# Kernel tuning notes

Hardware: AMD Instinct MI355X
Metric: run time of the kernel (lower is better)

Reference implementation:

```python
import jax, jax.numpy as jnp
import numpy as np

N_NODES = 50000
N_EDGES = 1600000
IN_C, HID_C, OUT_C = 64, 64, 7


def setup_inputs() -> dict:
    key = jax.random.key(0)
    ks = jax.random.split(key, 8)
    x = jax.random.normal(ks[0], (N_NODES, IN_C), dtype=jnp.float32)
    edge_index = jax.random.randint(ks[1], (2, N_EDGES), 0, N_NODES, dtype=jnp.int64)
    s_in = 1.0 / np.sqrt(IN_C)
    s_hid = 1.0 / np.sqrt(HID_C)
    W1 = jax.random.normal(ks[2], (HID_C, IN_C), dtype=jnp.float32) * s_in
    b1 = jnp.zeros((HID_C,), dtype=jnp.float32)
    W2 = jax.random.normal(ks[3], (HID_C, HID_C), dtype=jnp.float32) * s_hid
    b2 = jnp.zeros((HID_C,), dtype=jnp.float32)
    W3 = jax.random.normal(ks[4], (OUT_C, HID_C), dtype=jnp.float32) * s_hid
    b3 = jnp.zeros((OUT_C,), dtype=jnp.float32)
    return {"x": x, "edge_index": edge_index, "W1": W1, "b1": b1,
            "W2": W2, "b2": b2, "W3": W3, "b3": b3}


def _gcn_conv(x, src, dst, W, b):
    # GCNConv(normalize=False): lin -> sum-aggregate over incoming edges -> +bias
    h = x @ W.T                                   # [N, out]
    msg = h[src]                                  # gather source features [E, out]
    agg = jax.ops.segment_sum(msg, dst, num_segments=N_NODES)  # scatter-add
    return agg + b


def reference(x, edge_index, W1, b1, W2, b2, W3, b3):
    src, dst = edge_index[0], edge_index[1]
    h = jax.nn.relu(_gcn_conv(x, src, dst, W1, b1))   # dropout is identity in eval
    h = jax.nn.relu(_gcn_conv(h, src, dst, W2, b2))
    h = _gcn_conv(h, src, dst, W3, b3)
    return jax.nn.log_softmax(h, axis=-1)
```

## Files before the change

### kernel.cpp

```cpp
#include <hip/hip_runtime.h>
#include <math.h>

#define N_NODES 50000
#define N_EDGES 1600000
#define C 64
#define OUTC 7

#define NB 196
#define BCAP 10240
#define CHUNK 8192

#define ZROW N_NODES

typedef __attribute__((ext_vector_type(8))) short bf16x8;
typedef __attribute__((ext_vector_type(4))) float f32x4;
typedef __attribute__((ext_vector_type(2))) float f32x2;

__device__ __forceinline__ unsigned int pk_bf16(float a, float b) {
    unsigned int ua = __float_as_uint(a);
    ua = (ua + 0x7FFFu + ((ua >> 16) & 1u)) >> 16;
    unsigned int ub = __float_as_uint(b);
    ub = (ub + 0x7FFFu + ((ub >> 16) & 1u)) >> 16;
    return ua | (ub << 16);
}

union U4B8 { uint4 u; bf16x8 s; };

__global__ __launch_bounds__(256) void prep(const float* __restrict__ W1,
                                            const float* __restrict__ W2,
                                            unsigned int* __restrict__ Wb1,
                                            unsigned int* __restrict__ Wb2,
                                            int* __restrict__ gcursor) {
    const int b = blockIdx.x;
    const int tid = threadIdx.x;
    if (b < 8) {
        int idx = b * 256 + tid;
        float2 v = ((const float2*)W1)[idx];
        Wb1[idx] = pk_bf16(v.x, v.y);
    } else if (b < 16) {
        int idx = (b - 8) * 256 + tid;
        float2 v = ((const float2*)W2)[idx];
        Wb2[idx] = pk_bf16(v.x, v.y);
    } else {
        if (tid < NB) gcursor[tid] = 0;
    }
}

__global__ __launch_bounds__(256) void bin_kernel(const int* __restrict__ src,
                                                  const int* __restrict__ dst,
                                                  unsigned int* __restrict__ buckets,
                                                  int* __restrict__ gcursor) {
    __shared__ unsigned int staged[CHUNK];
    __shared__ int hist[NB], scanb[NB], cur[NB], baseb[NB];
    const int tid = threadIdx.x;
    const int base = blockIdx.x * CHUNK;
    int n = N_EDGES - base; if (n > CHUNK) n = CHUNK;

    for (int b = tid; b < NB; b += 256) { hist[b] = 0; cur[b] = 0; }
    __syncthreads();

    const int4* src4 = (const int4*)(src + base);
    const int4* dst4 = (const int4*)(dst + base);
    unsigned int v[32];
    int nv = n >> 2;
#pragma unroll
    for (int k = 0; k < 8; ++k) {
        int i4 = k * 256 + tid;
        if (i4 < nv) {
            int4 s4 = src4[i4];
            int4 d4 = dst4[i4];
            unsigned int d0 = (unsigned int)d4.x, d1 = (unsigned int)d4.y;
            unsigned int d2 = (unsigned int)d4.z, d3 = (unsigned int)d4.w;
            v[k * 4 + 0] = (d0 << 16) | (unsigned int)s4.x;
            v[k * 4 + 1] = (d1 << 16) | (unsigned int)s4.y;
            v[k * 4 + 2] = (d2 << 16) | (unsigned int)s4.z;
            v[k * 4 + 3] = (d3 << 16) | (unsigned int)s4.w;
            atomicAdd(&hist[d0 >> 8], 1);
            atomicAdd(&hist[d1 >> 8], 1);
            atomicAdd(&hist[d2 >> 8], 1);
            atomicAdd(&hist[d3 >> 8], 1);
        }
    }
    __syncthreads();
    if (tid == 0) {
        int run = 0;
        for (int b = 0; b < NB; ++b) { scanb[b] = run; run += hist[b]; }
    }
    __syncthreads();
#pragma unroll
    for (int k = 0; k < 8; ++k) {
        int i4 = k * 256 + tid;
        if (i4 < nv) {
#pragma unroll
            for (int q = 0; q < 4; ++q) {
                unsigned int w = v[k * 4 + q];
                int b = w >> 24;
                int p = scanb[b] + atomicAdd(&cur[b], 1);
                staged[p] = w;
            }
        }
    }
    __syncthreads();
    if (tid < NB) baseb[tid] = atomicAdd(&gcursor[tid], hist[tid]);
    __syncthreads();
    for (int i = tid; i < n; i += 256) {
        unsigned int w = staged[i];
        int b = w >> 24;
        buckets[(size_t)b * BCAP + baseb[b] + (i - scanb[b])] = w;
    }
}

__global__ __launch_bounds__(256) void build_csr(const unsigned int* __restrict__ buckets,
                                                 const int* __restrict__ gcursor,
                                                 unsigned int* __restrict__ csr,
                                                 int* __restrict__ off) {
    __shared__ int hist[256], part[256], offx[256], cur[256];
    __shared__ int gl[NB];
    __shared__ int s_cnt, s_base;
    const int tid = threadIdx.x;
    const int b = blockIdx.x;

    hist[tid] = 0;
    cur[tid] = 0;
    if (tid < NB) gl[tid] = gcursor[tid];
    __syncthreads();
    if (tid == 0) {
        int bs = 0;
        for (int i = 0; i < b; ++i) bs += gl[i];
        s_base = bs;
        s_cnt = gl[b];
    }
    __syncthreads();
    const int cnt = s_cnt;
    const int gbase = s_base;
    const unsigned int* bk = buckets + (size_t)b * BCAP;

    for (int i = tid; i < cnt; i += 256) {
        atomicAdd(&hist[(bk[i] >> 16) & 255], 1);
    }
    __syncthreads();
    part[tid] = hist[tid];
    __syncthreads();
    for (int d = 1; d < 256; d <<= 1) {
        int t = (tid >= d) ? part[tid - d] : 0;
        __syncthreads();
        part[tid] += t;
        __syncthreads();
    }
    offx[tid] = (tid == 0) ? 0 : part[tid - 1];
    __syncthreads();
    int node = b * 256 + tid;
    if (node < N_NODES) off[node] = gbase + offx[tid];
    if (b == NB - 1 && tid == 0) off[N_NODES] = gbase + cnt;
    for (int i = tid; i < cnt; i += 256) {
        unsigned int w = bk[i];
        int dl = (w >> 16) & 255;
        int p = offx[dl] + atomicAdd(&cur[dl], 1);
        csr[gbase + p] = w & 0xFFFFu;
    }
}


__global__ __launch_bounds__(256) void linear64_mfma_x(const float* __restrict__ x,
                                                       const unsigned int* __restrict__ Wb,
                                                       unsigned int* __restrict__ out) {
    if (blockIdx.x == 0 && threadIdx.x < 32)
        out[(size_t)ZROW * 32 + threadIdx.x] = 0u;
    const int wave = threadIdx.x >> 6;
    const int lane = threadIdx.x & 63;
    const int quad = lane >> 4;
    const int l16  = lane & 15;
    const int rbase = blockIdx.x * 64 + wave * 16;
    if (rbase >= N_NODES) return;

    U4B8 bfrag[4][2];
#pragma unroll
    for (int ct = 0; ct < 4; ++ct)
#pragma unroll
        for (int kt = 0; kt < 2; ++kt)
            bfrag[ct][kt].u = *(const uint4*)(Wb + (ct * 16 + l16) * 32 + kt * 16 + quad * 4);

    U4B8 afrag[2];
#pragma unroll
    for (int kt = 0; kt < 2; ++kt) {
        const float4* xp = (const float4*)(x + (size_t)(rbase + l16) * 64 + kt * 32 + quad * 8);
        float4 f0 = xp[0];
        float4 f1 = xp[1];
        afrag[kt].u.x = pk_bf16(f0.x, f0.y);
        afrag[kt].u.y = pk_bf16(f0.z, f0.w);
        afrag[kt].u.z = pk_bf16(f1.x, f1.y);
        afrag[kt].u.w = pk_bf16(f1.z, f1.w);
    }

    f32x4 acc[4];
#pragma unroll
    for (int ct = 0; ct < 4; ++ct) {
        f32x4 z = {0.f, 0.f, 0.f, 0.f};
        z = __builtin_amdgcn_mfma_f32_16x16x32_bf16(afrag[0].s, bfrag[ct][0].s, z, 0, 0, 0);
        z = __builtin_amdgcn_mfma_f32_16x16x32_bf16(afrag[1].s, bfrag[ct][1].s, z, 0, 0, 0);
        acc[ct] = z;
    }

    const int colp = l16 >> 1;
    const bool even = (l16 & 1) == 0;
#pragma unroll
    for (int ct = 0; ct < 4; ++ct) {
#pragma unroll
        for (int i = 0; i < 4; ++i) {
            float v = acc[ct][i];
            float p = __shfl_xor(v, 1, 64);
            if (even) {
                int row = rbase + quad * 4 + i;
                out[(size_t)row * 32 + ct * 8 + colp] = pk_bf16(v, p);
            }
        }
    }
}

__global__ __launch_bounds__(256) void linear64_mfma(const unsigned int* __restrict__ in,
                                                     const unsigned int* __restrict__ Wb,
                                                     unsigned int* __restrict__ out) {
    if (blockIdx.x == 0 && threadIdx.x < 32)
        out[(size_t)ZROW * 32 + threadIdx.x] = 0u;
    const int wave = threadIdx.x >> 6;
    const int lane = threadIdx.x & 63;
    const int quad = lane >> 4;
    const int l16  = lane & 15;
    const int rbase = blockIdx.x * 64 + wave * 16;
    if (rbase >= N_NODES) return;

    U4B8 bfrag[4][2];
#pragma unroll
    for (int ct = 0; ct < 4; ++ct)
#pragma unroll
        for (int kt = 0; kt < 2; ++kt)
            bfrag[ct][kt].u = *(const uint4*)(Wb + (ct * 16 + l16) * 32 + kt * 16 + quad * 4);

    U4B8 afrag[2];
#pragma unroll
    for (int kt = 0; kt < 2; ++kt)
        afrag[kt].u = *(const uint4*)(in + (size_t)(rbase + l16) * 32 + kt * 16 + quad * 4);

    f32x4 acc[4];
#pragma unroll
    for (int ct = 0; ct < 4; ++ct) {
        f32x4 z = {0.f, 0.f, 0.f, 0.f};
        z = __builtin_amdgcn_mfma_f32_16x16x32_bf16(afrag[0].s, bfrag[ct][0].s, z, 0, 0, 0);
        z = __builtin_amdgcn_mfma_f32_16x16x32_bf16(afrag[1].s, bfrag[ct][1].s, z, 0, 0, 0);
        acc[ct] = z;
    }

    const int colp = l16 >> 1;
    const bool even = (l16 & 1) == 0;
#pragma unroll
    for (int ct = 0; ct < 4; ++ct) {
#pragma unroll
        for (int i = 0; i < 4; ++i) {
            float v = acc[ct][i];
            float p = __shfl_xor(v, 1, 64);
            if (even) {
                int row = rbase + quad * 4 + i;
                out[(size_t)row * 32 + ct * 8 + colp] = pk_bf16(v, p);
            }
        }
    }
}

#define ACC8(v)                                                              \
    do {                                                                     \
        s01 += (f32x2){__uint_as_float((v).x << 16),                         \
                       __uint_as_float((v).x & 0xFFFF0000u)};                \
        s23 += (f32x2){__uint_as_float((v).y << 16),                         \
                       __uint_as_float((v).y & 0xFFFF0000u)};                \
        s45 += (f32x2){__uint_as_float((v).z << 16),                         \
                       __uint_as_float((v).z & 0xFFFF0000u)};                \
        s67 += (f32x2){__uint_as_float((v).w << 16),                         \
                       __uint_as_float((v).w & 0xFFFF0000u)};                \
    } while (0)

__global__ __launch_bounds__(256) void gather64b(const int* __restrict__ off,
                                                 const unsigned int* __restrict__ csr_src,
                                                 const unsigned int* __restrict__ tb,
                                                 const float* __restrict__ b,
                                                 unsigned int* __restrict__ hb) {
    int node = blockIdx.x * 4 + (threadIdx.x >> 6);
    if (node >= N_NODES) return;
    const int lane = threadIdx.x & 63;
    const int slot = lane >> 3;
    const int ch8  = lane & 7;
    int e0 = off[node], e1 = off[node + 1];
    const uint4* t4 = (const uint4*)tb;
    f32x2 s01 = {0.f, 0.f}, s23 = {0.f, 0.f}, s45 = {0.f, 0.f}, s67 = {0.f, 0.f};
    for (int e = e0; e < e1; e += 32) {
        int i0 = e + slot, i1 = i0 + 8, i2 = i0 + 16, i3 = i0 + 24;
        unsigned int a0 = csr_src[i0];
        unsigned int a1 = csr_src[i1];
        unsigned int a2 = csr_src[i2];
        unsigned int a3 = csr_src[i3];
        a0 = (i0 < e1) ? a0 : ZROW;
        a1 = (i1 < e1) ? a1 : ZROW;
        a2 = (i2 < e1) ? a2 : ZROW;
        a3 = (i3 < e1) ? a3 : ZROW;
        uint4 v0 = t4[(size_t)a0 * 8 + ch8];
        uint4 v1 = t4[(size_t)a1 * 8 + ch8];
        uint4 v2 = t4[(size_t)a2 * 8 + ch8];
        uint4 v3 = t4[(size_t)a3 * 8 + ch8];
        ACC8(v0);
        ACC8(v1);
        ACC8(v2);
        ACC8(v3);
    }
    float s[8] = {s01.x, s01.y, s23.x, s23.y, s45.x, s45.y, s67.x, s67.y};
#pragma unroll
    for (int d = 8; d <= 32; d <<= 1) {
#pragma unroll
        for (int j = 0; j < 8; ++j) s[j] += __shfl_xor(s[j], d, 64);
    }
    if (lane < 8) {
        const float4 b0 = ((const float4*)b)[ch8 * 2];
        const float4 b1 = ((const float4*)b)[ch8 * 2 + 1];
        float r0 = fmaxf(s[0] + b0.x, 0.f);
        float r1 = fmaxf(s[1] + b0.y, 0.f);
        float r2 = fmaxf(s[2] + b0.z, 0.f);
        float r3 = fmaxf(s[3] + b0.w, 0.f);
        float r4 = fmaxf(s[4] + b1.x, 0.f);
        float r5 = fmaxf(s[5] + b1.y, 0.f);
        float r6 = fmaxf(s[6] + b1.z, 0.f);
        float r7 = fmaxf(s[7] + b1.w, 0.f);
        uint4 w;
        w.x = pk_bf16(r0, r1);
        w.y = pk_bf16(r2, r3);
        w.z = pk_bf16(r4, r5);
        w.w = pk_bf16(r6, r7);
        ((uint4*)(hb + (size_t)node * 32))[ch8] = w;
    }
}

__global__ __launch_bounds__(256) void gather64b_w3(const int* __restrict__ off,
                                                    const unsigned int* __restrict__ csr_src,
                                                    const unsigned int* __restrict__ tb,
                                                    const float* __restrict__ b,
                                                    const float* __restrict__ W3,
                                                    unsigned int* __restrict__ t3) {
    int node = blockIdx.x * 4 + (threadIdx.x >> 6);
    if (node >= N_NODES) return;
    const int lane = threadIdx.x & 63;
    const int slot = lane >> 3;
    const int ch8  = lane & 7;
    int e0 = off[node], e1 = off[node + 1];
    const uint4* t4 = (const uint4*)tb;
    f32x2 s01 = {0.f, 0.f}, s23 = {0.f, 0.f}, s45 = {0.f, 0.f}, s67 = {0.f, 0.f};
    for (int e = e0; e < e1; e += 32) {
        int i0 = e + slot, i1 = i0 + 8, i2 = i0 + 16, i3 = i0 + 24;
        unsigned int a0 = csr_src[i0];
        unsigned int a1 = csr_src[i1];
        unsigned int a2 = csr_src[i2];
        unsigned int a3 = csr_src[i3];
        a0 = (i0 < e1) ? a0 : ZROW;
        a1 = (i1 < e1) ? a1 : ZROW;
        a2 = (i2 < e1) ? a2 : ZROW;
        a3 = (i3 < e1) ? a3 : ZROW;
        uint4 v0 = t4[(size_t)a0 * 8 + ch8];
        uint4 v1 = t4[(size_t)a1 * 8 + ch8];
        uint4 v2 = t4[(size_t)a2 * 8 + ch8];
        uint4 v3 = t4[(size_t)a3 * 8 + ch8];
        ACC8(v0);
        ACC8(v1);
        ACC8(v2);
        ACC8(v3);
    }
    float s[8] = {s01.x, s01.y, s23.x, s23.y, s45.x, s45.y, s67.x, s67.y};
#pragma unroll
    for (int d = 8; d <= 32; d <<= 1) {
#pragma unroll
        for (int j = 0; j < 8; ++j) s[j] += __shfl_xor(s[j], d, 64);
    }
    const float4 b0 = ((const float4*)b)[ch8 * 2];
    const float4 b1 = ((const float4*)b)[ch8 * 2 + 1];
    float r[8];
    r[0] = fmaxf(s[0] + b0.x, 0.f);
    r[1] = fmaxf(s[1] + b0.y, 0.f);
    r[2] = fmaxf(s[2] + b0.z, 0.f);
    r[3] = fmaxf(s[3] + b0.w, 0.f);
    r[4] = fmaxf(s[4] + b1.x, 0.f);
    r[5] = fmaxf(s[5] + b1.y, 0.f);
    r[6] = fmaxf(s[6] + b1.z, 0.f);
    r[7] = fmaxf(s[7] + b1.w, 0.f);
    float p[7];
#pragma unroll
    for (int j = 0; j < 7; ++j) {
        const float4 wa = *(const float4*)(W3 + j * 64 + ch8 * 8);
        const float4 wb = *(const float4*)(W3 + j * 64 + ch8 * 8 + 4);
        float t = r[0] * wa.x + r[1] * wa.y + r[2] * wa.z + r[3] * wa.w
                + r[4] * wb.x + r[5] * wb.y + r[6] * wb.z + r[7] * wb.w;
        t += __shfl_xor(t, 1, 64);
        t += __shfl_xor(t, 2, 64);
        t += __shfl_xor(t, 4, 64);
        p[j] = t;
    }
    if (lane == 0) {
        uint4 w;
        w.x = pk_bf16(p[0], p[1]);
        w.y = pk_bf16(p[2], p[3]);
        w.z = pk_bf16(p[4], p[5]);
        w.w = pk_bf16(p[6], 0.f);
        *(uint4*)(t3 + (size_t)node * 4) = w;
    }
}

__global__ __launch_bounds__(256) void gather7_lsm(const int* __restrict__ off,
                                                   const unsigned int* __restrict__ csr_src,
                                                   const unsigned int* __restrict__ t3,
                                                   const float* __restrict__ b,
                                                   float* __restrict__ out) {
    int node = blockIdx.x * 4 + (threadIdx.x >> 6);
    if (node >= N_NODES) return;
    const int lane = threadIdx.x & 63;
    const int slot = lane >> 1;
    const int h    = lane & 1;
    int e0 = off[node], e1 = off[node + 1];
    const uint2* t2 = (const uint2*)t3;
    float sx = 0.f, sy = 0.f, sz = 0.f, sw = 0.f;
    for (int e = e0 + slot; e < e1; e += 32) {
        unsigned int s = csr_src[e];
        uint2 v = t2[(size_t)s * 2 + h];
        sx += __uint_as_float(v.x << 16);
        sy += __uint_as_float(v.x & 0xFFFF0000u);
        sz += __uint_as_float(v.y << 16);
        sw += __uint_as_float(v.y & 0xFFFF0000u);
    }
#pragma unroll
    for (int d = 2; d <= 32; d <<= 1) {
        sx += __shfl_xor(sx, d, 64); sy += __shfl_xor(sy, d, 64);
        sz += __shfl_xor(sz, d, 64); sw += __shfl_xor(sw, d, 64);
    }
    float z0 = sx + b[h * 4 + 0];
    float z1 = sy + b[h * 4 + 1];
    float z2 = sz + b[h * 4 + 2];
    float z3 = (h == 0) ? (sw + b[3]) : -1e30f;
    float m = fmaxf(fmaxf(z0, z1), fmaxf(z2, z3));
    m = fmaxf(m, __shfl_xor(m, 1, 64));
    float ex = __expf(z0 - m) + __expf(z1 - m) + __expf(z2 - m) + __expf(z3 - m);
    ex += __shfl_xor(ex, 1, 64);
    float l = m + __logf(ex);
    if (lane < 2) {
        float* o = out + (size_t)node * 7 + h * 4;
        o[0] = z0 - l; o[1] = z1 - l; o[2] = z2 - l;
        if (h == 0) o[3] = z3 - l;
    }
}

extern "C" void kernel_launch(void* const* d_in, const int* in_sizes, int n_in,
                              void* d_out, int out_size, void* d_ws, size_t ws_size,
                              hipStream_t stream) {
    const float* x  = (const float*)d_in[0];
    const int*   ei = (const int*)d_in[1];
    const float* W1 = (const float*)d_in[2];
    const float* b1 = (const float*)d_in[3];
    const float* W2 = (const float*)d_in[4];
    const float* b2 = (const float*)d_in[5];
    const float* W3 = (const float*)d_in[6];
    const float* b3 = (const float*)d_in[7];
    float* out = (float*)d_out;

    const int* src = ei;
    const int* dst = ei + N_EDGES;

    float* A = (float*)d_ws;
    float* B = A + (size_t)N_NODES * C;
    unsigned int* csr = (unsigned int*)(B + (size_t)N_NODES * C);
    int* off     = (int*)(csr + N_EDGES);
    int* gcursor = off + N_NODES + 8;
    unsigned int* Wb1 = (unsigned int*)(gcursor + 256);
    unsigned int* Wb2 = Wb1 + 2048;
    unsigned int* buckets = (unsigned int*)A;
    unsigned int* Abf     = (unsigned int*)A;
    unsigned int* Hbf     = (unsigned int*)B;
    unsigned int* T3      = (unsigned int*)B;

    const int mfmagrid = (N_NODES + 63) / 64;
    const int ngrid    = (N_NODES + 3) / 4;

    prep<<<17, 256, 0, stream>>>(W1, W2, Wb1, Wb2, gcursor);

    bin_kernel<<<(N_EDGES + CHUNK - 1) / CHUNK, 256, 0, stream>>>(src, dst, buckets, gcursor);
    build_csr<<<NB, 256, 0, stream>>>(buckets, gcursor, csr, off);

    linear64_mfma_x<<<mfmagrid, 256, 0, stream>>>(x, Wb1, Abf);
    gather64b<<<ngrid, 256, 0, stream>>>(off, csr, Abf, b1, Hbf);

    linear64_mfma<<<mfmagrid, 256, 0, stream>>>(Hbf, Wb2, Abf);

    gather64b_w3<<<ngrid, 256, 0, stream>>>(off, csr, Abf, b2, W3, T3);

    gather7_lsm<<<ngrid, 256, 0, stream>>>(off, csr, T3, b3, out);
}
```

Baseline: 217.5 us.

## Split bf16 feature tables into column halves for cache-resident gathers

Splits each 64-channel bf16 node feature table into two 32-channel half-tables and runs each gather pass separately per half. This shrinks the randomly gathered working set (about 3.2 MB per half) so it fits better in L2/MALL, at the cost of reading the CSR twice and launching more kernels. The W3 projection is now accumulated with float atomics into a zeroed fp32 buffer, which adds a memset and atomics, and gather7 reads fp32 instead of bf16.

```diff
diff --git a/kernel.cpp b/kernel.cpp
--- a/kernel.cpp
+++ b/kernel.cpp
@@ -11,10 +11,12 @@
 #define CHUNK 8192
 
 #define ZROW N_NODES
+#define HROW 16
 
 typedef __attribute__((ext_vector_type(8))) short bf16x8;
 typedef __attribute__((ext_vector_type(4))) float f32x4;
 typedef __attribute__((ext_vector_type(2))) float f32x2;
+typedef __attribute__((ext_vector_type(4))) unsigned int u32x4;
 
 __device__ __forceinline__ unsigned int pk_bf16(float a, float b) {
     unsigned int ua = __float_as_uint(a);
@@ -163,9 +165,12 @@
 
 __global__ __launch_bounds__(256) void linear64_mfma_x(const float* __restrict__ x,
                                                        const unsigned int* __restrict__ Wb,
-                                                       unsigned int* __restrict__ out) {
-    if (blockIdx.x == 0 && threadIdx.x < 32)
-        out[(size_t)ZROW * 32 + threadIdx.x] = 0u;
+                                                       unsigned int* __restrict__ outA,
+                                                       unsigned int* __restrict__ outB) {
+    if (blockIdx.x == 0 && threadIdx.x < 16) {
+        outA[(size_t)ZROW * HROW + threadIdx.x] = 0u;
+        outB[(size_t)ZROW * HROW + threadIdx.x] = 0u;
+    }
     const int wave = threadIdx.x >> 6;
     const int lane = threadIdx.x & 63;
     const int quad = lane >> 4;
@@ -205,23 +210,29 @@
     const bool even = (l16 & 1) == 0;
 #pragma unroll
     for (int ct = 0; ct < 4; ++ct) {
+        unsigned int* outh = (ct < 2) ? outA : outB;
+        const int cg = (ct & 1) * 8 + colp;
 #pragma unroll
         for (int i = 0; i < 4; ++i) {
             float v = acc[ct][i];
             float p = __shfl_xor(v, 1, 64);
             if (even) {
                 int row = rbase + quad * 4 + i;
-                out[(size_t)row * 32 + ct * 8 + colp] = pk_bf16(v, p);
+                outh[(size_t)row * HROW + cg] = pk_bf16(v, p);
             }
         }
     }
 }
 
-__global__ __launch_bounds__(256) void linear64_mfma(const unsigned int* __restrict__ in,
+__global__ __launch_bounds__(256) void linear64_mfma(const unsigned int* __restrict__ inA,
+                                                     const unsigned int* __restrict__ inB,
                                                      const unsigned int* __restrict__ Wb,
-                                                     unsigned int* __restrict__ out) {
-    if (blockIdx.x == 0 && threadIdx.x < 32)
-        out[(size_t)ZROW * 32 + threadIdx.x] = 0u;
+                                                     unsigned int* __restrict__ outA,
+                                                     unsigned int* __restrict__ outB) {
+    if (blockIdx.x == 0 && threadIdx.x < 16) {
+        outA[(size_t)ZROW * HROW + threadIdx.x] = 0u;
+        outB[(size_t)ZROW * HROW + threadIdx.x] = 0u;
+    }
     const int wave = threadIdx.x >> 6;
     const int lane = threadIdx.x & 63;
     const int quad = lane >> 4;
@@ -237,9 +248,8 @@
             bfrag[ct][kt].u = *(const uint4*)(Wb + (ct * 16 + l16) * 32 + kt * 16 + quad * 4);
 
     U4B8 afrag[2];
-#pragma unroll
-    for (int kt = 0; kt < 2; ++kt)
-        afrag[kt].u = *(const uint4*)(in + (size_t)(rbase + l16) * 32 + kt * 16 + quad * 4);
+    afrag[0].u = *(const uint4*)(inA + (size_t)(rbase + l16) * HROW + quad * 4);
+    afrag[1].u = *(const uint4*)(inB + (size_t)(rbase + l16) * HROW + quad * 4);
 
     f32x4 acc[4];
 #pragma unroll
@@ -254,163 +264,139 @@
     const bool even = (l16 & 1) == 0;
 #pragma unroll
     for (int ct = 0; ct < 4; ++ct) {
+        unsigned int* outh = (ct < 2) ? outA : outB;
+        const int cg = (ct & 1) * 8 + colp;
 #pragma unroll
         for (int i = 0; i < 4; ++i) {
             float v = acc[ct][i];
             float p = __shfl_xor(v, 1, 64);
             if (even) {
                 int row = rbase + quad * 4 + i;
-                out[(size_t)row * 32 + ct * 8 + colp] = pk_bf16(v, p);
+                outh[(size_t)row * HROW + cg] = pk_bf16(v, p);
             }
         }
     }
 }
 
-#define ACC8(v)                                                              \
+#define ACCQ(v)                                                              \
     do {                                                                     \
-        s01 += (f32x2){__uint_as_float((v).x << 16),                         \
-                       __uint_as_float((v).x & 0xFFFF0000u)};                \
-        s23 += (f32x2){__uint_as_float((v).y << 16),                         \
-                       __uint_as_float((v).y & 0xFFFF0000u)};                \
-        s45 += (f32x2){__uint_as_float((v).z << 16),                         \
-                       __uint_as_float((v).z & 0xFFFF0000u)};                \
-        s67 += (f32x2){__uint_as_float((v).w << 16),                         \
-                       __uint_as_float((v).w & 0xFFFF0000u)};                \
+        q0 += (f32x2){__uint_as_float((v).x << 16),                          \
+                      __uint_as_float((v).x & 0xFFFF0000u)};                 \
+        q1 += (f32x2){__uint_as_float((v).y << 16),                          \
+                      __uint_as_float((v).y & 0xFFFF0000u)};                 \
+        q2 += (f32x2){__uint_as_float((v).z << 16),                          \
+                      __uint_as_float((v).z & 0xFFFF0000u)};                 \
+        q3 += (f32x2){__uint_as_float((v).w << 16),                          \
+                      __uint_as_float((v).w & 0xFFFF0000u)};                 \
     } while (0)
 
-__global__ __launch_bounds__(256) void gather64b(const int* __restrict__ off,
-                                                 const unsigned int* __restrict__ csr_src,
-                                                 const unsigned int* __restrict__ tb,
-                                                 const float* __restrict__ b,
-                                                 unsigned int* __restrict__ hb) {
+#define QREDUCE()                                                            \
+    do {                                                                     \
+        _Pragma("unroll")                                                    \
+        for (int d = 4; d <= 32; d <<= 1) {                                  \
+            q0.x += __shfl_xor(q0.x, d, 64); q0.y += __shfl_xor(q0.y, d, 64);\
+            q1.x += __shfl_xor(q1.x, d, 64); q1.y += __shfl_xor(q1.y, d, 64);\
+            q2.x += __shfl_xor(q2.x, d, 64); q2.y += __shfl_xor(q2.y, d, 64);\
+            q3.x += __shfl_xor(q3.x, d, 64); q3.y += __shfl_xor(q3.y, d, 64);\
+        }                                                                    \
+    } while (0)
+
+__global__ __launch_bounds__(256) void gather_h_half(const int* __restrict__ off,
+                                                     const unsigned int* __restrict__ csr_src,
+                                                     const unsigned int* __restrict__ th,
+                                                     const float* __restrict__ b,
+                                                     unsigned int* __restrict__ hh,
+                                                     int half) {
     int node = blockIdx.x * 4 + (threadIdx.x >> 6);
     if (node >= N_NODES) return;
     const int lane = threadIdx.x & 63;
-    const int slot = lane >> 3;
-    const int ch8  = lane & 7;
+    const int slot = lane >> 2;
+    const int ln   = lane & 3;
     int e0 = off[node], e1 = off[node + 1];
-    const uint4* t4 = (const uint4*)tb;
-    f32x2 s01 = {0.f, 0.f}, s23 = {0.f, 0.f}, s45 = {0.f, 0.f}, s67 = {0.f, 0.f};
+    const uint4* t4 = (const uint4*)th;
+    f32x2 q0 = {0.f, 0.f}, q1 = {0.f, 0.f}, q2 = {0.f, 0.f}, q3 = {0.f, 0.f};
     for (int e = e0; e < e1; e += 32) {
-        int i0 = e + slot, i1 = i0 + 8, i2 = i0 + 16, i3 = i0 + 24;
+        int i0 = e + slot, i1 = i0 + 16;
         unsigned int a0 = csr_src[i0];
         unsigned int a1 = csr_src[i1];
-        unsigned int a2 = csr_src[i2];
-        unsigned int a3 = csr_src[i3];
         a0 = (i0 < e1) ? a0 : ZROW;
         a1 = (i1 < e1) ? a1 : ZROW;
-        a2 = (i2 < e1) ? a2 : ZROW;
-        a3 = (i3 < e1) ? a3 : ZROW;
-        uint4 v0 = t4[(size_t)a0 * 8 + ch8];
-        uint4 v1 = t4[(size_t)a1 * 8 + ch8];
-        uint4 v2 = t4[(size_t)a2 * 8 + ch8];
-        uint4 v3 = t4[(size_t)a3 * 8 + ch8];
-        ACC8(v0);
-        ACC8(v1);
-        ACC8(v2);
-        ACC8(v3);
-    }
-    float s[8] = {s01.x, s01.y, s23.x, s23.y, s45.x, s45.y, s67.x, s67.y};
-#pragma unroll
-    for (int d = 8; d <= 32; d <<= 1) {
-#pragma unroll
-        for (int j = 0; j < 8; ++j) s[j] += __shfl_xor(s[j], d, 64);
-    }
-    if (lane < 8) {
-        const float4 b0 = ((const float4*)b)[ch8 * 2];
-        const float4 b1 = ((const float4*)b)[ch8 * 2 + 1];
-        float r0 = fmaxf(s[0] + b0.x, 0.f);
-        float r1 = fmaxf(s[1] + b0.y, 0.f);
-        float r2 = fmaxf(s[2] + b0.z, 0.f);
-        float r3 = fmaxf(s[3] + b0.w, 0.f);
-        float r4 = fmaxf(s[4] + b1.x, 0.f);
-        float r5 = fmaxf(s[5] + b1.y, 0.f);
-        float r6 = fmaxf(s[6] + b1.z, 0.f);
-        float r7 = fmaxf(s[7] + b1.w, 0.f);
-        uint4 w;
+        uint4 v0 = t4[(size_t)a0 * 4 + ln];
+        uint4 v1 = t4[(size_t)a1 * 4 + ln];
+        ACCQ(v0);
+        ACCQ(v1);
+    }
+    QREDUCE();
+    if (lane < 4) {
+        const int cb = half * 32 + ln * 8;
+        float r0 = fmaxf(q0.x + b[cb + 0], 0.f);
+        float r1 = fmaxf(q0.y + b[cb + 1], 0.f);
+        float r2 = fmaxf(q1.x + b[cb + 2], 0.f);
+        float r3 = fmaxf(q1.y + b[cb + 3], 0.f);
+        float r4 = fmaxf(q2.x + b[cb + 4], 0.f);
+        float r5 = fmaxf(q2.y + b[cb + 5], 0.f);
+        float r6 = fmaxf(q3.x + b[cb + 6], 0.f);
+        float r7 = fmaxf(q3.y + b[cb + 7], 0.f);
+        u32x4 w;
         w.x = pk_bf16(r0, r1);
         w.y = pk_bf16(r2, r3);
         w.z = pk_bf16(r4, r5);
         w.w = pk_bf16(r6, r7);
-        ((uint4*)(hb + (size_t)node * 32))[ch8] = w;
-    }
-}
-
-__global__ __launch_bounds__(256) void gather64b_w3(const int* __restrict__ off,
-                                                    const unsigned int* __restrict__ csr_src,
-                                                    const unsigned int* __restrict__ tb,
-                                                    const float* __restrict__ b,
-                                                    const float* __restrict__ W3,
-                                                    unsigned int* __restrict__ t3) {
+        __builtin_nontemporal_store(w, (u32x4*)(hh + (size_t)node * HROW) + ln);
+    }
+}
+
+__global__ __launch_bounds__(256) void gather_w3_half(const int* __restrict__ off,
+                                                      const unsigned int* __restrict__ csr_src,
+                                                      const unsigned int* __restrict__ th,
+                                                      const float* __restrict__ b,
+                                                      const float* __restrict__ W3,
+                                                      float* __restrict__ t3f,
+                                                      int half) {
     int node = blockIdx.x * 4 + (threadIdx.x >> 6);
     if (node >= N_NODES) return;
     const int lane = threadIdx.x & 63;
-    const int slot = lane >> 3;
-    const int ch8  = lane & 7;
+    const int slot = lane >> 2;
+    const int ln   = lane & 3;
     int e0 = off[node], e1 = off[node + 1];
-    const uint4* t4 = (const uint4*)tb;
-    f32x2 s01 = {0.f, 0.f}, s23 = {0.f, 0.f}, s45 = {0.f, 0.f}, s67 = {0.f, 0.f};
+    const uint4* t4 = (const uint4*)th;
+    f32x2 q0 = {0.f, 0.f}, q1 = {0.f, 0.f}, q2 = {0.f, 0.f}, q3 = {0.f, 0.f};
     for (int e = e0; e < e1; e += 32) {
-        int i0 = e + slot, i1 = i0 + 8, i2 = i0 + 16, i3 = i0 + 24;
+        int i0 = e + slot, i1 = i0 + 16;
         unsigned int a0 = csr_src[i0];
         unsigned int a1 = csr_src[i1];
-        unsigned int a2 = csr_src[i2];
-        unsigned int a3 = csr_src[i3];
         a0 = (i0 < e1) ? a0 : ZROW;
         a1 = (i1 < e1) ? a1 : ZROW;
-        a2 = (i2 < e1) ? a2 : ZROW;
-        a3 = (i3 < e1) ? a3 : ZROW;
-        uint4 v0 = t4[(size_t)a0 * 8 + ch8];
-        uint4 v1 = t4[(size_t)a1 * 8 + ch8];
-        uint4 v2 = t4[(size_t)a2 * 8 + ch8];
-        uint4 v3 = t4[(size_t)a3 * 8 + ch8];
-        ACC8(v0);
-        ACC8(v1);
-        ACC8(v2);
-        ACC8(v3);
-    }
-    float s[8] = {s01.x, s01.y, s23.x, s23.y, s45.x, s45.y, s67.x, s67.y};
-#pragma unroll
-    for (int d = 8; d <= 32; d <<= 1) {
-#pragma unroll
-        for (int j = 0; j < 8; ++j) s[j] += __shfl_xor(s[j], d, 64);
-    }
-    const float4 b0 = ((const float4*)b)[ch8 * 2];
-    const float4 b1 = ((const float4*)b)[ch8 * 2 + 1];
-    float r[8];
-    r[0] = fmaxf(s[0] + b0.x, 0.f);
-    r[1] = fmaxf(s[1] + b0.y, 0.f);
-    r[2] = fmaxf(s[2] + b0.z, 0.f);
-    r[3] = fmaxf(s[3] + b0.w, 0.f);
-    r[4] = fmaxf(s[4] + b1.x, 0.f);
-    r[5] = fmaxf(s[5] + b1.y, 0.f);
-    r[6] = fmaxf(s[6] + b1.z, 0.f);
-    r[7] = fmaxf(s[7] + b1.w, 0.f);
-    float p[7];
+        uint4 v0 = t4[(size_t)a0 * 4 + ln];
+        uint4 v1 = t4[(size_t)a1 * 4 + ln];
+        ACCQ(v0);
+        ACCQ(v1);
+    }
+    QREDUCE();
+    const int cb = half * 32 + ln * 8;
+    float r0 = fmaxf(q0.x + b[cb + 0], 0.f);
+    float r1 = fmaxf(q0.y + b[cb + 1], 0.f);
+    float r2 = fmaxf(q1.x + b[cb + 2], 0.f);
+    float r3 = fmaxf(q1.y + b[cb + 3], 0.f);
+    float r4 = fmaxf(q2.x + b[cb + 4], 0.f);
+    float r5 = fmaxf(q2.y + b[cb + 5], 0.f);
+    float r6 = fmaxf(q3.x + b[cb + 6], 0.f);
+    float r7 = fmaxf(q3.y + b[cb + 7], 0.f);
 #pragma unroll
     for (int j = 0; j < 7; ++j) {
-        const float4 wa = *(const float4*)(W3 + j * 64 + ch8 * 8);
-        const float4 wb = *(const float4*)(W3 + j * 64 + ch8 * 8 + 4);
-        float t = r[0] * wa.x + r[1] * wa.y + r[2] * wa.z + r[3] * wa.w
-                + r[4] * wb.x + r[5] * wb.y + r[6] * wb.z + r[7] * wb.w;
+        const float4 wa = *(const float4*)(W3 + j * 64 + cb);
+        const float4 wb = *(const float4*)(W3 + j * 64 + cb + 4);
+        float t = r0 * wa.x + r1 * wa.y + r2 * wa.z + r3 * wa.w
+                + r4 * wb.x + r5 * wb.y + r6 * wb.z + r7 * wb.w;
         t += __shfl_xor(t, 1, 64);
         t += __shfl_xor(t, 2, 64);
-        t += __shfl_xor(t, 4, 64);
-        p[j] = t;
-    }
-    if (lane == 0) {
-        uint4 w;
-        w.x = pk_bf16(p[0], p[1]);
-        w.y = pk_bf16(p[2], p[3]);
-        w.z = pk_bf16(p[4], p[5]);
-        w.w = pk_bf16(p[6], 0.f);
-        *(uint4*)(t3 + (size_t)node * 4) = w;
+        if (lane == 0) atomicAdd(t3f + (size_t)node * 8 + j, t);
     }
 }
 
 __global__ __launch_bounds__(256) void gather7_lsm(const int* __restrict__ off,
                                                    const unsigned int* __restrict__ csr_src,
-                                                   const unsigned int* __restrict__ t3,
+                                                   const float* __restrict__ t3f,
                                                    const float* __restrict__ b,
                                                    float* __restrict__ out) {
     int node = blockIdx.x * 4 + (threadIdx.x >> 6);
@@ -419,15 +405,12 @@
     const int slot = lane >> 1;
     const int h    = lane & 1;
     int e0 = off[node], e1 = off[node + 1];
-    const uint2* t2 = (const uint2*)t3;
+    const float4* t4 = (const float4*)t3f;
     float sx = 0.f, sy = 0.f, sz = 0.f, sw = 0.f;
     for (int e = e0 + slot; e < e1; e += 32) {
-        unsigned int s = csr_src[e];
-        uint2 v = t2[(size_t)s * 2 + h];
-        sx += __uint_as_float(v.x << 16);
-        sy += __uint_as_float(v.x & 0xFFFF0000u);
-        sz += __uint_as_float(v.y << 16);
-        sw += __uint_as_float(v.y & 0xFFFF0000u);
+        unsigned int a = csr_src[e];
+        float4 v = t4[(size_t)a * 2 + h];
+        sx += v.x; sy += v.y; sz += v.z; sw += v.w;
     }
 #pragma unroll
     for (int d = 2; d <= 32; d <<= 1) {
@@ -466,32 +449,36 @@
     const int* src = ei;
     const int* dst = ei + N_EDGES;
 
-    float* A = (float*)d_ws;
-    float* B = A + (size_t)N_NODES * C;
-    unsigned int* csr = (unsigned int*)(B + (size_t)N_NODES * C);
+    const size_t HT = (size_t)(N_NODES + 1) * HROW;
+    unsigned int* tA = (unsigned int*)d_ws;
+    unsigned int* tB = tA + HT;
+    unsigned int* hA = tB + HT;
+    unsigned int* hB = hA + HT;
+    float* t3f = (float*)(hB + HT);
+    unsigned int* csr = (unsigned int*)(t3f + (size_t)(N_NODES + 1) * 8);
     int* off     = (int*)(csr + N_EDGES);
     int* gcursor = off + N_NODES + 8;
     unsigned int* Wb1 = (unsigned int*)(gcursor + 256);
     unsigned int* Wb2 = Wb1 + 2048;
-    unsigned int* buckets = (unsigned int*)A;
-    unsigned int* Abf     = (unsigned int*)A;
-    unsigned int* Hbf     = (unsigned int*)B;
-    unsigned int* T3      = (unsigned int*)B;
+    unsigned int* buckets = tA;
 
     const int mfmagrid = (N_NODES + 63) / 64;
     const int ngrid    = (N_NODES + 3) / 4;
 
+    (void)hipMemsetAsync(t3f, 0, (size_t)(N_NODES + 1) * 8 * sizeof(float), stream);
     prep<<<17, 256, 0, stream>>>(W1, W2, Wb1, Wb2, gcursor);
 
     bin_kernel<<<(N_EDGES + CHUNK - 1) / CHUNK, 256, 0, stream>>>(src, dst, buckets, gcursor);
     build_csr<<<NB, 256, 0, stream>>>(buckets, gcursor, csr, off);
 
-    linear64_mfma_x<<<mfmagrid, 256, 0, stream>>>(x, Wb1, Abf);
-    gather64b<<<ngrid, 256, 0, stream>>>(off, csr, Abf, b1, Hbf);
-
-    linear64_mfma<<<mfmagrid, 256, 0, stream>>>(Hbf, Wb2, Abf);
-
-    gather64b_w3<<<ngrid, 256, 0, stream>>>(off, csr, Abf, b2, W3, T3);
-
-    gather7_lsm<<<ngrid, 256, 0, stream>>>(off, csr, T3, b3, out);
-}
+    linear64_mfma_x<<<mfmagrid, 256, 0, stream>>>(x, Wb1, tA, tB);
+    gather_h_half<<<ngrid, 256, 0, stream>>>(off, csr, tA, b1, hA, 0);
+    gather_h_half<<<ngrid, 256, 0, stream>>>(off, csr, tB, b1, hB, 1);
+
+    linear64_mfma<<<mfmagrid, 256, 0, stream>>>(hA, hB, Wb2, tA, tB);
+
+    gather_w3_half<<<ngrid, 256, 0, stream>>>(off, csr, tA, b2, W3, t3f, 0);
+    gather_w3_half<<<ngrid, 256, 0, stream>>>(off, csr, tB, b2, W3, t3f, 1);
+
+    gather7_lsm<<<ngrid, 256, 0, stream>>>(off, csr, t3f, b3, out);
+}
```

Measured after the change: 283.5 us. 1.3x slower.

## Fuse edge binning with layer-1 linear and fold W2 into first gather

Applied to the files above, without the earlier changes.

Merges the edge-binning kernel and the first MFMA linear layer into one launch by splitting blocks by role, so they can run concurrently. The second linear layer is folded into the first gather's epilogue as a per-node fp32 matvec with shuffle reductions, which removes a kernel and a round trip of the hidden features through memory. The last gather is unrolled two edges at a time, with tail lanes padded to a zero row. The cost is extra ALU and W2 loads in the gather kernel, plus more code to keep the zero rows and buffer placement correct.

```diff
diff --git a/kernel.cpp b/kernel.cpp
--- a/kernel.cpp
+++ b/kernel.cpp
@@ -9,6 +9,7 @@
 #define NB 196
 #define BCAP 10240
 #define CHUNK 8192
+#define BINBLKS 196
 
 #define ZROW N_NODES
 
@@ -27,9 +28,7 @@
 union U4B8 { uint4 u; bf16x8 s; };
 
 __global__ __launch_bounds__(256) void prep(const float* __restrict__ W1,
-                                            const float* __restrict__ W2,
                                             unsigned int* __restrict__ Wb1,
-                                            unsigned int* __restrict__ Wb2,
                                             int* __restrict__ gcursor) {
     const int b = blockIdx.x;
     const int tid = threadIdx.x;
@@ -37,76 +36,133 @@
         int idx = b * 256 + tid;
         float2 v = ((const float2*)W1)[idx];
         Wb1[idx] = pk_bf16(v.x, v.y);
-    } else if (b < 16) {
-        int idx = (b - 8) * 256 + tid;
-        float2 v = ((const float2*)W2)[idx];
-        Wb2[idx] = pk_bf16(v.x, v.y);
     } else {
         if (tid < NB) gcursor[tid] = 0;
     }
 }
 
-__global__ __launch_bounds__(256) void bin_kernel(const int* __restrict__ src,
-                                                  const int* __restrict__ dst,
-                                                  unsigned int* __restrict__ buckets,
-                                                  int* __restrict__ gcursor) {
+__global__ __launch_bounds__(256) void bin_lin1(const int* __restrict__ src,
+                                                const int* __restrict__ dst,
+                                                unsigned int* __restrict__ buckets,
+                                                int* __restrict__ gcursor,
+                                                const float* __restrict__ x,
+                                                const unsigned int* __restrict__ Wb,
+                                                unsigned int* __restrict__ tout) {
     __shared__ unsigned int staged[CHUNK];
     __shared__ int hist[NB], scanb[NB], cur[NB], baseb[NB];
     const int tid = threadIdx.x;
-    const int base = blockIdx.x * CHUNK;
-    int n = N_EDGES - base; if (n > CHUNK) n = CHUNK;
-
-    for (int b = tid; b < NB; b += 256) { hist[b] = 0; cur[b] = 0; }
-    __syncthreads();
-
-    const int4* src4 = (const int4*)(src + base);
-    const int4* dst4 = (const int4*)(dst + base);
-    unsigned int v[32];
-    int nv = n >> 2;
-#pragma unroll
-    for (int k = 0; k < 8; ++k) {
-        int i4 = k * 256 + tid;
-        if (i4 < nv) {
-            int4 s4 = src4[i4];
-            int4 d4 = dst4[i4];
-            unsigned int d0 = (unsigned int)d4.x, d1 = (unsigned int)d4.y;
-            unsigned int d2 = (unsigned int)d4.z, d3 = (unsigned int)d4.w;
-            v[k * 4 + 0] = (d0 << 16) | (unsigned int)s4.x;
-            v[k * 4 + 1] = (d1 << 16) | (unsigned int)s4.y;
-            v[k * 4 + 2] = (d2 << 16) | (unsigned int)s4.z;
-            v[k * 4 + 3] = (d3 << 16) | (unsigned int)s4.w;
-            atomicAdd(&hist[d0 >> 8], 1);
-            atomicAdd(&hist[d1 >> 8], 1);
-            atomicAdd(&hist[d2 >> 8], 1);
-            atomicAdd(&hist[d3 >> 8], 1);
-        }
-    }
-    __syncthreads();
-    if (tid == 0) {
-        int run = 0;
-        for (int b = 0; b < NB; ++b) { scanb[b] = run; run += hist[b]; }
-    }
-    __syncthreads();
-#pragma unroll
-    for (int k = 0; k < 8; ++k) {
-        int i4 = k * 256 + tid;
-        if (i4 < nv) {
-#pragma unroll
-            for (int q = 0; q < 4; ++q) {
-                unsigned int w = v[k * 4 + q];
-                int b = w >> 24;
-                int p = scanb[b] + atomicAdd(&cur[b], 1);
-                staged[p] = w;
+
+    if (blockIdx.x < BINBLKS) {
+        const int bx = blockIdx.x;
+        const int base = bx * CHUNK;
+        int n = N_EDGES - base; if (n > CHUNK) n = CHUNK;
+
+        for (int b = tid; b < NB; b += 256) { hist[b] = 0; cur[b] = 0; }
+        __syncthreads();
+
+        const int4* src4 = (const int4*)(src + base);
+        const int4* dst4 = (const int4*)(dst + base);
+        unsigned int v[32];
+        int nv = n >> 2;
+#pragma unroll
+        for (int k = 0; k < 8; ++k) {
+            int i4 = k * 256 + tid;
+            if (i4 < nv) {
+                int4 s4 = src4[i4];
+                int4 d4 = dst4[i4];
+                unsigned int d0 = (unsigned int)d4.x, d1 = (unsigned int)d4.y;
+                unsigned int d2 = (unsigned int)d4.z, d3 = (unsigned int)d4.w;
+                v[k * 4 + 0] = (d0 << 16) | (unsigned int)s4.x;
+                v[k * 4 + 1] = (d1 << 16) | (unsigned int)s4.y;
+                v[k * 4 + 2] = (d2 << 16) | (unsigned int)s4.z;
+                v[k * 4 + 3] = (d3 << 16) | (unsigned int)s4.w;
+                atomicAdd(&hist[d0 >> 8], 1);
+                atomicAdd(&hist[d1 >> 8], 1);
+                atomicAdd(&hist[d2 >> 8], 1);
+                atomicAdd(&hist[d3 >> 8], 1);
             }
         }
-    }
-    __syncthreads();
-    if (tid < NB) baseb[tid] = atomicAdd(&gcursor[tid], hist[tid]);
-    __syncthreads();
-    for (int i = tid; i < n; i += 256) {
-        unsigned int w = staged[i];
-        int b = w >> 24;
-        buckets[(size_t)b * BCAP + baseb[b] + (i - scanb[b])] = w;
+        __syncthreads();
+        if (tid == 0) {
+            int run = 0;
+            for (int b = 0; b < NB; ++b) { scanb[b] = run; run += hist[b]; }
+        }
+        __syncthreads();
+#pragma unroll
+        for (int k = 0; k < 8; ++k) {
+            int i4 = k * 256 + tid;
+            if (i4 < nv) {
+#pragma unroll
+                for (int q = 0; q < 4; ++q) {
+                    unsigned int w = v[k * 4 + q];
+                    int b = w >> 24;
+                    int p = scanb[b] + atomicAdd(&cur[b], 1);
+                    staged[p] = w;
+                }
+            }
+        }
+        __syncthreads();
+        if (tid < NB) baseb[tid] = atomicAdd(&gcursor[tid], hist[tid]);
+        __syncthreads();
+        for (int i = tid; i < n; i += 256) {
+            unsigned int w = staged[i];
+            int b = w >> 24;
+            buckets[(size_t)b * BCAP + baseb[b] + (i - scanb[b])] = w;
+        }
+        return;
+    }
+
+    const int bx = blockIdx.x - BINBLKS;
+    if (bx == 0 && tid < 32)
+        tout[(size_t)ZROW * 32 + tid] = 0u;
+    const int wave = tid >> 6;
+    const int lane = tid & 63;
+    const int quad = lane >> 4;
+    const int l16  = lane & 15;
+    const int rbase = bx * 64 + wave * 16;
+    if (rbase >= N_NODES) return;
+
+    U4B8 bfrag[4][2];
+#pragma unroll
+    for (int ct = 0; ct < 4; ++ct)
+#pragma unroll
+        for (int kt = 0; kt < 2; ++kt)
+            bfrag[ct][kt].u = *(const uint4*)(Wb + (ct * 16 + l16) * 32 + kt * 16 + quad * 4);
+
+    U4B8 afrag[2];
+#pragma unroll
+    for (int kt = 0; kt < 2; ++kt) {
+        const float4* xp = (const float4*)(x + (size_t)(rbase + l16) * 64 + kt * 32 + quad * 8);
+        float4 f0 = xp[0];
+        float4 f1 = xp[1];
+        afrag[kt].u.x = pk_bf16(f0.x, f0.y);
+        afrag[kt].u.y = pk_bf16(f0.z, f0.w);
+        afrag[kt].u.z = pk_bf16(f1.x, f1.y);
+        afrag[kt].u.w = pk_bf16(f1.z, f1.w);
+    }
+
+    f32x4 acc[4];
+#pragma unroll
+    for (int ct = 0; ct < 4; ++ct) {
+        f32x4 z = {0.f, 0.f, 0.f, 0.f};
+        z = __builtin_amdgcn_mfma_f32_16x16x32_bf16(afrag[0].s, bfrag[ct][0].s, z, 0, 0, 0);
+        z = __builtin_amdgcn_mfma_f32_16x16x32_bf16(afrag[1].s, bfrag[ct][1].s, z, 0, 0, 0);
+        acc[ct] = z;
+    }
+
+    const int colp = l16 >> 1;
+    const bool even = (l16 & 1) == 0;
+#pragma unroll
+    for (int ct = 0; ct < 4; ++ct) {
+#pragma unroll
+        for (int i = 0; i < 4; ++i) {
+            float v = acc[ct][i];
+            float p = __shfl_xor(v, 1, 64);
+            if (even) {
+                int row = rbase + quad * 4 + i;
+                tout[(size_t)row * 32 + ct * 8 + colp] = pk_bf16(v, p);
+            }
+        }
     }
 }
 
@@ -157,112 +213,6 @@
         int dl = (w >> 16) & 255;
         int p = offx[dl] + atomicAdd(&cur[dl], 1);
         csr[gbase + p] = w & 0xFFFFu;
-    }
-}
-
-
-__global__ __launch_bounds__(256) void linear64_mfma_x(const float* __restrict__ x,
-                                                       const unsigned int* __restrict__ Wb,
-                                                       unsigned int* __restrict__ out) {
-    if (blockIdx.x == 0 && threadIdx.x < 32)
-        out[(size_t)ZROW * 32 + threadIdx.x] = 0u;
-    const int wave = threadIdx.x >> 6;
-    const int lane = threadIdx.x & 63;
-    const int quad = lane >> 4;
-    const int l16  = lane & 15;
-    const int rbase = blockIdx.x * 64 + wave * 16;
-    if (rbase >= N_NODES) return;
-
-    U4B8 bfrag[4][2];
-#pragma unroll
-    for (int ct = 0; ct < 4; ++ct)
-#pragma unroll
-        for (int kt = 0; kt < 2; ++kt)
-            bfrag[ct][kt].u = *(const uint4*)(Wb + (ct * 16 + l16) * 32 + kt * 16 + quad * 4);
-
-    U4B8 afrag[2];
-#pragma unroll
-    for (int kt = 0; kt < 2; ++kt) {
-        const float4* xp = (const float4*)(x + (size_t)(rbase + l16) * 64 + kt * 32 + quad * 8);
-        float4 f0 = xp[0];
-        float4 f1 = xp[1];
-        afrag[kt].u.x = pk_bf16(f0.x, f0.y);
-        afrag[kt].u.y = pk_bf16(f0.z, f0.w);
-        afrag[kt].u.z = pk_bf16(f1.x, f1.y);
-        afrag[kt].u.w = pk_bf16(f1.z, f1.w);
-    }
-
-    f32x4 acc[4];
-#pragma unroll
-    for (int ct = 0; ct < 4; ++ct) {
-        f32x4 z = {0.f, 0.f, 0.f, 0.f};
-        z = __builtin_amdgcn_mfma_f32_16x16x32_bf16(afrag[0].s, bfrag[ct][0].s, z, 0, 0, 0);
-        z = __builtin_amdgcn_mfma_f32_16x16x32_bf16(afrag[1].s, bfrag[ct][1].s, z, 0, 0, 0);
-        acc[ct] = z;
-    }
-
-    const int colp = l16 >> 1;
-    const bool even = (l16 & 1) == 0;
-#pragma unroll
-    for (int ct = 0; ct < 4; ++ct) {
-#pragma unroll
-        for (int i = 0; i < 4; ++i) {
-            float v = acc[ct][i];
-            float p = __shfl_xor(v, 1, 64);
-            if (even) {
-                int row = rbase + quad * 4 + i;
-                out[(size_t)row * 32 + ct * 8 + colp] = pk_bf16(v, p);
-            }
-        }
-    }
-}
-
-__global__ __launch_bounds__(256) void linear64_mfma(const unsigned int* __restrict__ in,
-                                                     const unsigned int* __restrict__ Wb,
-                                                     unsigned int* __restrict__ out) {
-    if (blockIdx.x == 0 && threadIdx.x < 32)
-        out[(size_t)ZROW * 32 + threadIdx.x] = 0u;
-    const int wave = threadIdx.x >> 6;
-    const int lane = threadIdx.x & 63;
-    const int quad = lane >> 4;
-    const int l16  = lane & 15;
-    const int rbase = blockIdx.x * 64 + wave * 16;
-    if (rbase >= N_NODES) return;
-
-    U4B8 bfrag[4][2];
-#pragma unroll
-    for (int ct = 0; ct < 4; ++ct)
-#pragma unroll
-        for (int kt = 0; kt < 2; ++kt)
-            bfrag[ct][kt].u = *(const uint4*)(Wb + (ct * 16 + l16) * 32 + kt * 16 + quad * 4);
-
-    U4B8 afrag[2];
-#pragma unroll
-    for (int kt = 0; kt < 2; ++kt)
-        afrag[kt].u = *(const uint4*)(in + (size_t)(rbase + l16) * 32 + kt * 16 + quad * 4);
-
-    f32x4 acc[4];
-#pragma unroll
-    for (int ct = 0; ct < 4; ++ct) {
-        f32x4 z = {0.f, 0.f, 0.f, 0.f};
-        z = __builtin_amdgcn_mfma_f32_16x16x32_bf16(afrag[0].s, bfrag[ct][0].s, z, 0, 0, 0);
-        z = __builtin_amdgcn_mfma_f32_16x16x32_bf16(afrag[1].s, bfrag[ct][1].s, z, 0, 0, 0);
-        acc[ct] = z;
-    }
-
-    const int colp = l16 >> 1;
-    const bool even = (l16 & 1) == 0;
-#pragma unroll
-    for (int ct = 0; ct < 4; ++ct) {
-#pragma unroll
-        for (int i = 0; i < 4; ++i) {
-            float v = acc[ct][i];
-            float p = __shfl_xor(v, 1, 64);
-            if (even) {
-                int row = rbase + quad * 4 + i;
-                out[(size_t)row * 32 + ct * 8 + colp] = pk_bf16(v, p);
-            }
-        }
     }
 }
 
@@ -278,11 +228,14 @@
                        __uint_as_float((v).w & 0xFFFF0000u)};                \
     } while (0)
 
-__global__ __launch_bounds__(256) void gather64b(const int* __restrict__ off,
-                                                 const unsigned int* __restrict__ csr_src,
-                                                 const unsigned int* __restrict__ tb,
-                                                 const float* __restrict__ b,
-                                                 unsigned int* __restrict__ hb) {
+__global__ __launch_bounds__(256) void gather64_lin2(const int* __restrict__ off,
+                                                     const unsigned int* __restrict__ csr_src,
+                                                     const unsigned int* __restrict__ tb,
+                                                     const float* __restrict__ b,
+                                                     const float* __restrict__ W2,
+                                                     unsigned int* __restrict__ t2) {
+    if (blockIdx.x == 0 && threadIdx.x < 32)
+        t2[(size_t)ZROW * 32 + threadIdx.x] = 0u;
     int node = blockIdx.x * 4 + (threadIdx.x >> 6);
     if (node >= N_NODES) return;
     const int lane = threadIdx.x & 63;
@@ -316,23 +269,37 @@
 #pragma unroll
         for (int j = 0; j < 8; ++j) s[j] += __shfl_xor(s[j], d, 64);
     }
-    if (lane < 8) {
-        const float4 b0 = ((const float4*)b)[ch8 * 2];
-        const float4 b1 = ((const float4*)b)[ch8 * 2 + 1];
-        float r0 = fmaxf(s[0] + b0.x, 0.f);
-        float r1 = fmaxf(s[1] + b0.y, 0.f);
-        float r2 = fmaxf(s[2] + b0.z, 0.f);
-        float r3 = fmaxf(s[3] + b0.w, 0.f);
-        float r4 = fmaxf(s[4] + b1.x, 0.f);
-        float r5 = fmaxf(s[5] + b1.y, 0.f);
-        float r6 = fmaxf(s[6] + b1.z, 0.f);
-        float r7 = fmaxf(s[7] + b1.w, 0.f);
+    const float4 b0 = ((const float4*)b)[ch8 * 2];
+    const float4 b1v = ((const float4*)b)[ch8 * 2 + 1];
+    float r[8];
+    r[0] = fmaxf(s[0] + b0.x, 0.f);
+    r[1] = fmaxf(s[1] + b0.y, 0.f);
+    r[2] = fmaxf(s[2] + b0.z, 0.f);
+    r[3] = fmaxf(s[3] + b0.w, 0.f);
+    r[4] = fmaxf(s[4] + b1v.x, 0.f);
+    r[5] = fmaxf(s[5] + b1v.y, 0.f);
+    r[6] = fmaxf(s[6] + b1v.z, 0.f);
+    r[7] = fmaxf(s[7] + b1v.w, 0.f);
+    float p[8];
+#pragma unroll
+    for (int n = 0; n < 8; ++n) {
+        const float* wrow = W2 + (slot * 8 + n) * 64 + ch8 * 8;
+        const float4 wa = *(const float4*)wrow;
+        const float4 wb = *(const float4*)(wrow + 4);
+        float t = r[0] * wa.x + r[1] * wa.y + r[2] * wa.z + r[3] * wa.w
+                + r[4] * wb.x + r[5] * wb.y + r[6] * wb.z + r[7] * wb.w;
+        t += __shfl_xor(t, 1, 64);
+        t += __shfl_xor(t, 2, 64);
+        t += __shfl_xor(t, 4, 64);
+        p[n] = t;
+    }
+    if (ch8 == 0) {
         uint4 w;
-        w.x = pk_bf16(r0, r1);
-        w.y = pk_bf16(r2, r3);
-        w.z = pk_bf16(r4, r5);
-        w.w = pk_bf16(r6, r7);
-        ((uint4*)(hb + (size_t)node * 32))[ch8] = w;
+        w.x = pk_bf16(p[0], p[1]);
+        w.y = pk_bf16(p[2], p[3]);
+        w.z = pk_bf16(p[4], p[5]);
+        w.w = pk_bf16(p[6], p[7]);
+        ((uint4*)(t2 + (size_t)node * 32))[slot] = w;
     }
 }
 
@@ -342,6 +309,8 @@
                                                     const float* __restrict__ b,
                                                     const float* __restrict__ W3,
                                                     unsigned int* __restrict__ t3) {
+    if (blockIdx.x == 0 && threadIdx.x < 4)
+        t3[(size_t)ZROW * 4 + threadIdx.x] = 0u;
     int node = blockIdx.x * 4 + (threadIdx.x >> 6);
     if (node >= N_NODES) return;
     const int lane = threadIdx.x & 63;
@@ -376,16 +345,16 @@
         for (int j = 0; j < 8; ++j) s[j] += __shfl_xor(s[j], d, 64);
     }
     const float4 b0 = ((const float4*)b)[ch8 * 2];
-    const float4 b1 = ((const float4*)b)[ch8 * 2 + 1];
+    const float4 b1v = ((const float4*)b)[ch8 * 2 + 1];
     float r[8];
     r[0] = fmaxf(s[0] + b0.x, 0.f);
     r[1] = fmaxf(s[1] + b0.y, 0.f);
     r[2] = fmaxf(s[2] + b0.z, 0.f);
     r[3] = fmaxf(s[3] + b0.w, 0.f);
-    r[4] = fmaxf(s[4] + b1.x, 0.f);
-    r[5] = fmaxf(s[5] + b1.y, 0.f);
-    r[6] = fmaxf(s[6] + b1.z, 0.f);
-    r[7] = fmaxf(s[7] + b1.w, 0.f);
+    r[4] = fmaxf(s[4] + b1v.x, 0.f);
+    r[5] = fmaxf(s[5] + b1v.y, 0.f);
+    r[6] = fmaxf(s[6] + b1v.z, 0.f);
+    r[7] = fmaxf(s[7] + b1v.w, 0.f);
     float p[7];
 #pragma unroll
     for (int j = 0; j < 7; ++j) {
@@ -421,13 +390,23 @@
     int e0 = off[node], e1 = off[node + 1];
     const uint2* t2 = (const uint2*)t3;
     float sx = 0.f, sy = 0.f, sz = 0.f, sw = 0.f;
-    for (int e = e0 + slot; e < e1; e += 32) {
-        unsigned int s = csr_src[e];
-        uint2 v = t2[(size_t)s * 2 + h];
-        sx += __uint_as_float(v.x << 16);
-        sy += __uint_as_float(v.x & 0xFFFF0000u);
-        sz += __uint_as_float(v.y << 16);
-        sw += __uint_as_float(v.y & 0xFFFF0000u);
+    for (int e = e0; e < e1; e += 64) {
+        int i0 = e + slot;
+        int i1 = e + 32 + slot;
+        unsigned int a0 = csr_src[i0];
+        unsigned int a1 = csr_src[i1];
+        a0 = (i0 < e1) ? a0 : ZROW;
+        a1 = (i1 < e1) ? a1 : ZROW;
+        uint2 v0 = t2[(size_t)a0 * 2 + h];
+        uint2 v1 = t2[(size_t)a1 * 2 + h];
+        sx += __uint_as_float(v0.x << 16);
+        sy += __uint_as_float(v0.x & 0xFFFF0000u);
+        sz += __uint_as_float(v0.y << 16);
+        sw += __uint_as_float(v0.y & 0xFFFF0000u);
+        sx += __uint_as_float(v1.x << 16);
+        sy += __uint_as_float(v1.x & 0xFFFF0000u);
+        sz += __uint_as_float(v1.y << 16);
+        sw += __uint_as_float(v1.y & 0xFFFF0000u);
     }
 #pragma unroll
     for (int d = 2; d <= 32; d <<= 1) {
@@ -472,26 +451,24 @@
     int* off     = (int*)(csr + N_EDGES);
     int* gcursor = off + N_NODES + 8;
     unsigned int* Wb1 = (unsigned int*)(gcursor + 256);
-    unsigned int* Wb2 = Wb1 + 2048;
     unsigned int* buckets = (unsigned int*)A;
-    unsigned int* Abf     = (unsigned int*)A;
-    unsigned int* Hbf     = (unsigned int*)B;
-    unsigned int* T3      = (unsigned int*)B;
+    unsigned int* T2 = (unsigned int*)A;
+    unsigned int* Tt = (unsigned int*)B;
+    unsigned int* T3 = Tt + (size_t)(N_NODES + 1) * 32;
 
     const int mfmagrid = (N_NODES + 63) / 64;
     const int ngrid    = (N_NODES + 3) / 4;
 
-    prep<<<17, 256, 0, stream>>>(W1, W2, Wb1, Wb2, gcursor);
-
-    bin_kernel<<<(N_EDGES + CHUNK - 1) / CHUNK, 256, 0, stream>>>(src, dst, buckets, gcursor);
+    prep<<<9, 256, 0, stream>>>(W1, Wb1, gcursor);
+
+    bin_lin1<<<BINBLKS + mfmagrid, 256, 0, stream>>>(src, dst, buckets, gcursor,
+                                                     x, Wb1, Tt);
+
     build_csr<<<NB, 256, 0, stream>>>(buckets, gcursor, csr, off);
 
-    linear64_mfma_x<<<mfmagrid, 256, 0, stream>>>(x, Wb1, Abf);
-    gather64b<<<ngrid, 256, 0, stream>>>(off, csr, Abf, b1, Hbf);
-
-    linear64_mfma<<<mfmagrid, 256, 0, stream>>>(Hbf, Wb2, Abf);
-
-    gather64b_w3<<<ngrid, 256, 0, stream>>>(off, csr, Abf, b2, W3, T3);
+    gather64_lin2<<<ngrid, 256, 0, stream>>>(off, csr, Tt, b1, W2, T2);
+
+    gather64b_w3<<<ngrid, 256, 0, stream>>>(off, csr, T2, b2, W3, T3);
 
     gather7_lsm<<<ngrid, 256, 0, stream>>>(off, csr, T3, b3, out);
 }
```

New measurement: 216.0 us, median of 2. About the same (-0.7%).
